# Kernel optimization log

Measured on AMD Instinct MI355X. Metric: run time of the kernel, lower is better.

The kernel has to match this reference:

```python
import jax, jax.numpy as jnp
import numpy as np

N_NODES = 100000
N_EDGES = 1600000
IN_DIM = 128
HID = 64
NUM_GRAPHS = 2048
NUM_CLASSES = 1


def setup_inputs() -> dict:
    key = jax.random.key(0)
    ks = jax.random.split(key, 16)
    x = jax.random.normal(ks[0], (N_NODES, IN_DIM), dtype=jnp.float32)
    edge_index = jax.random.randint(ks[1], (2, N_EDGES), 0, N_NODES, dtype=jnp.int64)
    batch_index = jnp.sort(jax.random.randint(ks[2], (N_NODES,), 0, NUM_GRAPHS, dtype=jnp.int64))
    # GCNConv weights (glorot-ish scale)
    def lin(k, fi, fo):
        return jax.random.normal(k, (fi, fo), dtype=jnp.float32) / np.sqrt(fi)
    W1 = lin(ks[3], IN_DIM, HID); b1 = jnp.zeros((HID,), jnp.float32)
    W2 = lin(ks[4], HID, HID);    b2 = jnp.zeros((HID,), jnp.float32)
    W3 = lin(ks[5], HID, HID);    b3 = jnp.zeros((HID,), jnp.float32)
    W4 = lin(ks[6], HID, HID);    b4 = jnp.zeros((HID,), jnp.float32)
    Wout = lin(ks[7], 2 * HID, NUM_CLASSES); bout = jnp.zeros((NUM_CLASSES,), jnp.float32)
    return {"x": x, "edge_index": edge_index, "batch_index": batch_index,
            "W1": W1, "b1": b1, "W2": W2, "b2": b2, "W3": W3, "b3": b3,
            "W4": W4, "b4": b4, "Wout": Wout, "bout": bout}


def _gcn_conv(x, W, b, src, dst, norm, n):
    # PyG GCNConv: linear transform, then D^-1/2 (A+I) D^-1/2 aggregation, then bias
    h = x @ W                                   # [N, F_out]
    msg = h[src] * norm[:, None]                # [E+N, F_out] gather + scale
    agg = jax.ops.segment_sum(msg, dst, num_segments=n)
    return agg + b


def reference(x, edge_index, batch_index, W1, b1, W2, b2, W3, b3, W4, b4, Wout, bout):
    n = x.shape[0]
    loops = jnp.arange(n, dtype=edge_index.dtype)
    src = jnp.concatenate([edge_index[0], loops])  # add self-loops
    dst = jnp.concatenate([edge_index[1], loops])
    deg = jax.ops.segment_sum(jnp.ones_like(dst, dtype=x.dtype), dst, num_segments=n)
    dis = jax.lax.rsqrt(deg)                       # deg >= 1 due to self-loops
    norm = dis[src] * dis[dst]

    h = x
    for (W, b) in ((W1, b1), (W2, b2), (W3, b3), (W4, b4)):
        h = jax.nn.relu(_gcn_conv(h, W, b, src, dst, norm, n))

    # global mean pool + global max pool per graph
    counts = jax.ops.segment_sum(jnp.ones((n,), h.dtype), batch_index, num_segments=NUM_GRAPHS)
    mean = jax.ops.segment_sum(h, batch_index, num_segments=NUM_GRAPHS) / jnp.maximum(counts, 1.0)[:, None]
    mx = jax.ops.segment_max(h, batch_index, num_segments=NUM_GRAPHS)
    mx = jnp.where(counts[:, None] > 0, mx, 0.0)
    pooled = jnp.concatenate([mean, mx], axis=1)   # [G, 2*HID]

    out = pooled @ Wout + bout                     # [G, 1]
    return (out, pooled)
```

## Files before the change

### kernel.cpp

```cpp
#include <hip/hip_runtime.h>
#include <hip/hip_fp16.h>

#define N_NODES 100000
#define IN_DIM 128
#define HID 64
#define NUM_GRAPHS 2048
#define CNE_MAX (1600000 + 7 * N_NODES)
#define BROWS 128
#define NBUCK ((N_NODES + BROWS - 1) / BROWS)
#define NCHUNK 256
#define TOTP (NBUCK * NCHUNK)
#define CAP 4096

typedef _Float16 h8 __attribute__((ext_vector_type(8)));
typedef float f4 __attribute__((ext_vector_type(4)));


__global__ __launch_bounds__(256) void hist_partial(const int* __restrict__ dst,
                                                    int* __restrict__ partial,
                                                    int E, int chunk,
                                                    unsigned* __restrict__ padA,
                                                    unsigned* __restrict__ padB) {
    __shared__ int lh[NBUCK];
    int t = threadIdx.x, c = blockIdx.x;
    if (c == 0) {
        if (t < 32) padA[t] = 0;
        else if (t < 64) padB[t - 32] = 0;
    }
    for (int b = t; b < NBUCK; b += 256) lh[b] = 0;
    __syncthreads();
    int lo = c * chunk, hi = min(lo + chunk, E);
    for (int i = lo + t; i < hi; i += 256) atomicAdd(&lh[dst[i] >> 7], 1);
    __syncthreads();
    for (int b = t; b < NBUCK; b += 256) partial[b * NCHUNK + c] = lh[b];
}

__global__ void scan1(const int* __restrict__ counts, int* __restrict__ out1,
                      int* __restrict__ bsum, int n, int pad8) {
    __shared__ int s[256];
    int t = threadIdx.x;
    int base = blockIdx.x * 1024 + t * 4;
    int v[4];
#pragma unroll
    for (int i = 0; i < 4; i++) {
        int c = (base + i < n) ? counts[base + i] : 0;
        v[i] = pad8 ? ((c + 7) & ~7) : c;
    }
    int tsum = v[0] + v[1] + v[2] + v[3];
    s[t] = tsum;
    __syncthreads();
    for (int off = 1; off < 256; off <<= 1) {
        int tv = (t >= off) ? s[t - off] : 0;
        __syncthreads();
        s[t] += tv;
        __syncthreads();
    }
    int excl = s[t] - tsum;
    if (t == 255) bsum[blockIdx.x] = s[255];
    int run = excl;
#pragma unroll
    for (int i = 0; i < 4; i++) {
        run += v[i];
        if (base + i < n) out1[base + i] = run;
    }
}

__device__ __forceinline__ int inline_bscan(const int* __restrict__ bsum, int nb, int* s) {
    int t = threadIdx.x;
    int v = (t < nb) ? bsum[t] : 0;
    s[t] = v;
    __syncthreads();
    for (int off = 1; off < 256; off <<= 1) {
        int tv = (t >= off) ? s[t - off] : 0;
        __syncthreads();
        s[t] += tv;
        __syncthreads();
    }
    int excl = s[t] - v;
    __syncthreads();
    s[t] = excl;
    __syncthreads();
    return excl;
}

__global__ __launch_bounds__(256) void scan3(int* __restrict__ row_ptr,
                                             const int* __restrict__ bsum, int nb, int n) {
    __shared__ int s[256];
    inline_bscan(bsum, nb, s);
    int i = blockIdx.x * blockDim.x + threadIdx.x;
    if (i == 0) row_ptr[0] = 0;
    if (i < n) row_ptr[i + 1] += s[i >> 10];
}

__global__ __launch_bounds__(256) void scan3p(const int* __restrict__ partial,
                                              const int* __restrict__ pincl,
                                              const int* __restrict__ bsum, int nb,
                                              int* __restrict__ base,
                                              int* __restrict__ part_off, int E) {
    __shared__ int s[256];
    inline_bscan(bsum, nb, s);
    int i = blockIdx.x * blockDim.x + threadIdx.x;
    if (i < TOTP) {
        int v = pincl[i] + s[i >> 10] - partial[i];
        base[i] = v;
        if ((i & (NCHUNK - 1)) == 0) part_off[i / NCHUNK] = v;
    }
    if (i == 0) part_off[NBUCK] = E;
}

__global__ __launch_bounds__(256) void partition_edges(const int* __restrict__ src,
                                                       const int* __restrict__ dst,
                                                       const int* __restrict__ base,
                                                       unsigned* __restrict__ part,
                                                       int E, int chunk) {
    __shared__ int cur[NBUCK];
    int t = threadIdx.x, c = blockIdx.x;
    for (int b = t; b < NBUCK; b += 256) cur[b] = base[b * NCHUNK + c];
    __syncthreads();
    int lo = c * chunk, hi = min(lo + chunk, E);
    for (int i = lo + t; i < hi; i += 256) {
        int s = src[i], d = dst[i];
        int pos = atomicAdd(&cur[d >> 7], 1);
        part[pos] = (unsigned)s | ((unsigned)(d & (BROWS - 1)) << 17);
    }
}

__global__ __launch_bounds__(256) void deg_dis(const unsigned* __restrict__ part,
                                               const int* __restrict__ part_off,
                                               int* __restrict__ pdeg,
                                               float* __restrict__ dis, int n) {
    __shared__ int cnt[BROWS];
    int t = threadIdx.x, b = blockIdx.x;
    int r0 = b * BROWS;
    if (t < BROWS) cnt[t] = 0;
    __syncthreads();
    for (int i = part_off[b] + t; i < part_off[b + 1]; i += 256)
        atomicAdd(&cnt[part[i] >> 17], 1);
    __syncthreads();
    int nrows = min(BROWS, n - r0);
    if (t < nrows) {
        int dg = cnt[t];
        pdeg[r0 + t] = dg;
        dis[r0 + t] = rsqrtf((float)(dg + 1));
    }
}

__global__ __launch_bounds__(256) void build_csr(const unsigned* __restrict__ part,
                                                 const int* __restrict__ part_off,
                                                 const int* __restrict__ row_ptr,
                                                 unsigned* __restrict__ cne, int n) {
    __shared__ int fill[BROWS];
    __shared__ unsigned stage[CAP];
    int b = blockIdx.x;
    int r0 = b * BROWS;
    int t = threadIdx.x;
    int nrows = min(BROWS, n - r0);
    int base = row_ptr[r0];
    int region = row_ptr[r0 + nrows] - base;
    for (int r = t; r < nrows; r += 256) fill[r] = row_ptr[r0 + r] - base;
    int i0 = part_off[b], i1 = part_off[b + 1];
    if (region <= CAP) {
        for (int i = t; i < region; i += 256) stage[i] = (unsigned)N_NODES << 7;
        __syncthreads();
        for (int i = i0 + t; i < i1; i += 256) {
            unsigned pe = part[i];
            int pos = atomicAdd(&fill[pe >> 17], 1);
            stage[pos] = (pe & 0x1FFFFu) << 7;
        }
        __syncthreads();
        for (int i = t; i < region; i += 256) cne[base + i] = stage[i];
    } else {
        for (int i = t; i < region; i += 256) cne[base + i] = (unsigned)N_NODES << 7;
        __syncthreads();
        for (int i = i0 + t; i < i1; i += 256) {
            unsigned pe = part[i];
            int pos = atomicAdd(&fill[pe >> 17], 1);
            cne[base + pos] = (pe & 0x1FFFFu) << 7;
        }
    }
}


template <int K, typename XT>
__global__ __launch_bounds__(256) void gemm_mfma(const XT* __restrict__ X,
                                                 const float* __restrict__ W,
                                                 const float* __restrict__ dis,
                                                 __half* __restrict__ out, int n) {
    const int KS = K / 32;
    int wave = threadIdx.x >> 6, lane = threadIdx.x & 63;
    int quad = lane >> 4, l16 = lane & 15;
    h8 b[4][KS];
#pragma unroll
    for (int ct = 0; ct < 4; ct++)
#pragma unroll
        for (int ks = 0; ks < KS; ks++)
#pragma unroll
            for (int j = 0; j < 8; j++)
                b[ct][ks][j] = (_Float16)W[(ks * 32 + quad * 8 + j) * HID + ct * 16 + l16];
    int ntile = n >> 4;
    int wpb = blockDim.x >> 6;
    int stride = gridDim.x * wpb;
    for (int rt = blockIdx.x * wpb + wave; rt < ntile; rt += stride) {
        int row0 = rt << 4;
        const XT* xr = X + (size_t)(row0 + l16) * K + quad * 8;
        f4 acc[4];
#pragma unroll
        for (int ct = 0; ct < 4; ct++) acc[ct] = (f4)(0.f);
#pragma unroll
        for (int ks = 0; ks < KS; ks++) {
            h8 a;
            if constexpr (__is_same(XT, float)) {
                float4 xa = *(const float4*)(xr + ks * 32);
                float4 xb = *(const float4*)(xr + ks * 32 + 4);
                a[0] = (_Float16)xa.x; a[1] = (_Float16)xa.y;
                a[2] = (_Float16)xa.z; a[3] = (_Float16)xa.w;
                a[4] = (_Float16)xb.x; a[5] = (_Float16)xb.y;
                a[6] = (_Float16)xb.z; a[7] = (_Float16)xb.w;
            } else {
                a = *(const h8*)(xr + ks * 32);
            }
#pragma unroll
            for (int ct = 0; ct < 4; ct++)
                acc[ct] = __builtin_amdgcn_mfma_f32_16x16x32_f16(a, b[ct][ks], acc[ct], 0, 0, 0);
        }
        int r0 = row0 + quad * 4;
        float4 dv = *(const float4*)(dis + r0);
        float dd[4] = {dv.x, dv.y, dv.z, dv.w};
#pragma unroll
        for (int reg = 0; reg < 4; reg++) {
            __half* orow = out + (size_t)(r0 + reg) * HID + l16;
            orow[0]  = __float2half(dd[reg] * acc[0][reg]);
            orow[16] = __float2half(dd[reg] * acc[1][reg]);
            orow[32] = __float2half(dd[reg] * acc[2][reg]);
            orow[48] = __float2half(dd[reg] * acc[3][reg]);
        }
    }
}

template <typename OutT>
__global__ __launch_bounds__(256) void aggregate2(const __half* __restrict__ tmp,
                                                  const float* __restrict__ dis,
                                                  const int* __restrict__ row_ptr,
                                                  const unsigned* __restrict__ cne,
                                                  const float* __restrict__ bias,
                                                  OutT* __restrict__ out, int n) {
    int wave = threadIdx.x >> 6, lane = threadIdx.x & 63;
    int m = lane & 31, hh = lane >> 5;
    const char* tbase = (const char*)tmp + 4 * m;
    int wpb = blockDim.x >> 6;
    int stride = gridDim.x * wpb;
    float2 blv = *(const float2*)(bias + 2 * m);
    int npairs = n >> 1;
    for (int p = blockIdx.x * wpb + wave; p < npairs; p += stride) {
        int row = 2 * p + hh;
        float dr = dis[row];
        int s = row_ptr[row], e = row_ptr[row + 1];
        int ng = (e - s) >> 3;
        float ax0 = 0.f, ay0 = 0.f, ax1 = 0.f, ay1 = 0.f;
        float ax2 = 0.f, ay2 = 0.f, ax3 = 0.f, ay3 = 0.f;
        if (ng > 0) {
            const uint4* ip = (const uint4*)(cne + s);
            uint4 A0 = ip[0], A1 = ip[1];
            __half2 g0 = *(const __half2*)(tbase + A0.x);
            __half2 g1 = *(const __half2*)(tbase + A0.y);
            __half2 g2 = *(const __half2*)(tbase + A0.z);
            __half2 g3 = *(const __half2*)(tbase + A0.w);
            __half2 g4 = *(const __half2*)(tbase + A1.x);
            __half2 g5 = *(const __half2*)(tbase + A1.y);
            __half2 g6 = *(const __half2*)(tbase + A1.z);
            __half2 g7 = *(const __half2*)(tbase + A1.w);
            uint4 B0, B1;
            if (ng > 1) { B0 = ip[2]; B1 = ip[3]; }
            for (int g = 1; g < ng; g++) {
                __half2 u0 = *(const __half2*)(tbase + B0.x);
                __half2 u1 = *(const __half2*)(tbase + B0.y);
                __half2 u2 = *(const __half2*)(tbase + B0.z);
                __half2 u3 = *(const __half2*)(tbase + B0.w);
                __half2 u4 = *(const __half2*)(tbase + B1.x);
                __half2 u5 = *(const __half2*)(tbase + B1.y);
                __half2 u6 = *(const __half2*)(tbase + B1.z);
                __half2 u7 = *(const __half2*)(tbase + B1.w);
                if (g + 1 < ng) { B0 = ip[2 * (g + 1)]; B1 = ip[2 * (g + 1) + 1]; }
                float2 f0 = __half22float2(g0), f1 = __half22float2(g1);
                float2 f2 = __half22float2(g2), f3 = __half22float2(g3);
                float2 f4 = __half22float2(g4), f5 = __half22float2(g5);
                float2 f6 = __half22float2(g6), f7 = __half22float2(g7);
                ax0 += f0.x; ay0 += f0.y; ax1 += f1.x; ay1 += f1.y;
                ax2 += f2.x; ay2 += f2.y; ax3 += f3.x; ay3 += f3.y;
                ax0 += f4.x; ay0 += f4.y; ax1 += f5.x; ay1 += f5.y;
                ax2 += f6.x; ay2 += f6.y; ax3 += f7.x; ay3 += f7.y;
                g0 = u0; g1 = u1; g2 = u2; g3 = u3;
                g4 = u4; g5 = u5; g6 = u6; g7 = u7;
            }
            float2 f0 = __half22float2(g0), f1 = __half22float2(g1);
            float2 f2 = __half22float2(g2), f3 = __half22float2(g3);
            float2 f4 = __half22float2(g4), f5 = __half22float2(g5);
            float2 f6 = __half22float2(g6), f7 = __half22float2(g7);
            ax0 += f0.x; ay0 += f0.y; ax1 += f1.x; ay1 += f1.y;
            ax2 += f2.x; ay2 += f2.y; ax3 += f3.x; ay3 += f3.y;
            ax0 += f4.x; ay0 += f4.y; ax1 += f5.x; ay1 += f5.y;
            ax2 += f6.x; ay2 += f6.y; ax3 += f7.x; ay3 += f7.y;
        }
        float sx = (ax0 + ax1) + (ax2 + ax3);
        float sy = (ay0 + ay1) + (ay2 + ay3);
        float2 selff = __half22float2(*(const __half2*)(tbase + (size_t)row * 128));
        float rx = fmaxf(dr * (selff.x + sx) + blv.x, 0.f);
        float ry = fmaxf(dr * (selff.y + sy) + blv.y, 0.f);
        if constexpr (__is_same(OutT, __half)) {
            *(__half2*)(out + (size_t)row * HID + 2 * m) = __floats2half2_rn(rx, ry);
        } else {
            *(float2*)(out + (size_t)row * HID + 2 * m) = make_float2(rx, ry);
        }
    }
}

__global__ __launch_bounds__(256) void pool_kernel(const float* __restrict__ h,
                                                   const int* __restrict__ batch,
                                                   const float* __restrict__ Wout,
                                                   const float* __restrict__ bout,
                                                   float* __restrict__ d_out, int n) {
    __shared__ float ssum[4][64];
    __shared__ float smax[4][64];
    int g = blockIdx.x;
    int wave = threadIdx.x >> 6, j = threadIdx.x & 63;
    int lo = 0, hi = n;
    while (lo < hi) { int mid = (lo + hi) >> 1; if (batch[mid] < g) lo = mid + 1; else hi = mid; }
    int start = lo;
    hi = n;
    while (lo < hi) { int mid = (lo + hi) >> 1; if (batch[mid] < g + 1) lo = mid + 1; else hi = mid; }
    int end = lo;

    float sum = 0.f, mx = 0.f;
    for (int i = start + wave; i < end; i += 4) {
        float v = h[(size_t)i * HID + j];
        sum += v;
        mx = fmaxf(mx, v);
    }
    ssum[wave][j] = sum;
    smax[wave][j] = mx;
    __syncthreads();
    if (wave == 0) {
        sum = (ssum[0][j] + ssum[1][j]) + (ssum[2][j] + ssum[3][j]);
        mx = fmaxf(fmaxf(smax[0][j], smax[1][j]), fmaxf(smax[2][j], smax[3][j]));
        float cnt = (float)(end - start);
        float mean = sum / fmaxf(cnt, 1.f);
        float* pooled = d_out + NUM_GRAPHS;
        pooled[(size_t)g * (2 * HID) + j] = mean;
        pooled[(size_t)g * (2 * HID) + HID + j] = mx;
        float c = mean * Wout[j] + mx * Wout[HID + j];
#pragma unroll
        for (int off = 32; off; off >>= 1) c += __shfl_down(c, off);
        if (j == 0) d_out[g] = c + bout[0];
    }
}


extern "C" void kernel_launch(void* const* d_in, const int* in_sizes, int n_in,
                              void* d_out, int out_size, void* d_ws, size_t ws_size,
                              hipStream_t stream) {
    const float* x    = (const float*)d_in[0];
    const int*   edge = (const int*)d_in[1];
    const int*   batch= (const int*)d_in[2];
    const float* W1 = (const float*)d_in[3];  const float* b1 = (const float*)d_in[4];
    const float* W2 = (const float*)d_in[5];  const float* b2 = (const float*)d_in[6];
    const float* W3 = (const float*)d_in[7];  const float* b3 = (const float*)d_in[8];
    const float* W4 = (const float*)d_in[9];  const float* b4 = (const float*)d_in[10];
    const float* Wout = (const float*)d_in[11]; const float* bout = (const float*)d_in[12];
    float* out = (float*)d_out;

    const int N = N_NODES;
    const int E = in_sizes[1] / 2;
    const int* src = edge;
    const int* dst = edge + E;
    const int chunk = (E + NCHUNK - 1) / NCHUNK;

    char* p = (char*)d_ws;
    auto alloc = [&](size_t bytes) -> char* {
        char* r = p;
        p += (bytes + 255) & ~(size_t)255;
        return r;
    };
    int*      pdeg     = (int*)alloc((size_t)N * 4);
    int*      row_ptr  = (int*)alloc((size_t)(N + 1) * 4);
    int*      partial  = (int*)alloc((size_t)TOTP * 4);
    int*      pincl    = (int*)alloc((size_t)TOTP * 4);
    int*      pbase    = (int*)alloc((size_t)TOTP * 4);
    int*      part_off = (int*)alloc((size_t)(NBUCK + 1) * 4);
    unsigned* part     = (unsigned*)alloc((size_t)1600000 * 4);
    unsigned* cne      = (unsigned*)alloc((size_t)CNE_MAX * 4);
    float*    dis      = (float*)alloc((size_t)N * 4);
    int*      bsum     = (int*)alloc(256 * 4);
    __half*   tmp      = (__half*)alloc((size_t)(N + 1) * HID * 2);
    float*    hA       = (float*)alloc((size_t)N * HID * 4);
    __half*   hH       = (__half*)hA;

    unsigned* padrow = (unsigned*)(tmp + (size_t)N * HID);
    hist_partial<<<NCHUNK, 256, 0, stream>>>(dst, partial, E, chunk, padrow, padrow);
    int nbp = (TOTP + 1023) / 1024;
    scan1<<<nbp, 256, 0, stream>>>(partial, pincl, bsum, TOTP, 0);
    scan3p<<<(TOTP + 255) / 256, 256, 0, stream>>>(partial, pincl, bsum, nbp, pbase, part_off, E);
    partition_edges<<<NCHUNK, 256, 0, stream>>>(src, dst, pbase, part, E, chunk);
    deg_dis<<<NBUCK, 256, 0, stream>>>(part, part_off, pdeg, dis, N);

    int nb = (N + 1023) / 1024;
    scan1<<<nb, 256, 0, stream>>>(pdeg, row_ptr + 1, bsum, N, 1);
    scan3<<<(N + 255) / 256, 256, 0, stream>>>(row_ptr, bsum, nb, N);
    build_csr<<<NBUCK, 256, 0, stream>>>(part, part_off, row_ptr, cne, N);

    const int AGG_BLOCKS = 2048;
    const int GEMM_BLOCKS = 1024;

    gemm_mfma<IN_DIM, float><<<GEMM_BLOCKS, 256, 0, stream>>>(x, W1, dis, tmp, N);
    aggregate2<__half><<<AGG_BLOCKS, 256, 0, stream>>>(tmp, dis, row_ptr, cne, b1, hH, N);
    gemm_mfma<HID, _Float16><<<GEMM_BLOCKS, 256, 0, stream>>>((_Float16*)hH, W2, dis, tmp, N);
    aggregate2<__half><<<AGG_BLOCKS, 256, 0, stream>>>(tmp, dis, row_ptr, cne, b2, hH, N);
    gemm_mfma<HID, _Float16><<<GEMM_BLOCKS, 256, 0, stream>>>((_Float16*)hH, W3, dis, tmp, N);
    aggregate2<__half><<<AGG_BLOCKS, 256, 0, stream>>>(tmp, dis, row_ptr, cne, b3, hH, N);
    gemm_mfma<HID, _Float16><<<GEMM_BLOCKS, 256, 0, stream>>>((_Float16*)hH, W4, dis, tmp, N);
    aggregate2<float><<<AGG_BLOCKS, 256, 0, stream>>>(tmp, dis, row_ptr, cne, b4, hA, N);

    pool_kernel<<<NUM_GRAPHS, 256, 0, stream>>>(hA, batch, Wout, bout, out, N);
}
```

Before: 343.2 us.

## Fuse GCN aggregation with next layer's MFMA GEMM via shared-memory tiles

Adds a kernel that aggregates 16 rows of neighbor features per wave, applies bias and ReLU, stages the fp16 result in swizzled LDS, then immediately multiplies by the next layer's weight with MFMA. This replaces three separate aggregate and GEMM launches, avoiding the intermediate hidden-state write and re-read to global memory plus the launch overheads. It uses ping-pong tmp buffers, and each lane now gathers 8 bytes covering 4 features with 16 lanes per row. This may reduce gather parallelism per row and occupancy compared with the standalone aggregate kernel.

```diff
diff --git a/kernel.cpp b/kernel.cpp
--- a/kernel.cpp
+++ b/kernel.cpp
@@ -14,6 +14,11 @@
 
 typedef _Float16 h8 __attribute__((ext_vector_type(8)));
 typedef float f4 __attribute__((ext_vector_type(4)));
+
+__device__ __forceinline__ float2 u2f2(unsigned u) {
+    __half2 h = *reinterpret_cast<__half2*>(&u);
+    return __half22float2(h);
+}
 
 
 __global__ __launch_bounds__(256) void hist_partial(const int* __restrict__ dst,
@@ -229,6 +234,121 @@
 #pragma unroll
         for (int reg = 0; reg < 4; reg++) {
             __half* orow = out + (size_t)(r0 + reg) * HID + l16;
+            orow[0]  = __float2half(dd[reg] * acc[0][reg]);
+            orow[16] = __float2half(dd[reg] * acc[1][reg]);
+            orow[32] = __float2half(dd[reg] * acc[2][reg]);
+            orow[48] = __float2half(dd[reg] * acc[3][reg]);
+        }
+    }
+}
+
+__global__ __launch_bounds__(256) void fused_agg_gemm2(const __half* __restrict__ tmp,
+                                                       const float* __restrict__ dis,
+                                                       const int* __restrict__ row_ptr,
+                                                       const unsigned* __restrict__ cne,
+                                                       const float* __restrict__ bias,
+                                                       const float* __restrict__ W,
+                                                       __half* __restrict__ out, int n) {
+    __shared__ __half hs[4][1024];
+    int wave = threadIdx.x >> 6, lane = threadIdx.x & 63;
+    int lr = lane >> 4, m4 = lane & 15;
+    int quad = lr, l16 = m4;
+    char* hsw = (char*)&hs[wave][0];
+    const char* tb = (const char*)tmp + 8 * m4;
+    float4 blv = *(const float4*)(bias + 4 * m4);
+    h8 bf[4][2];
+#pragma unroll
+    for (int ct = 0; ct < 4; ct++)
+#pragma unroll
+        for (int ks = 0; ks < 2; ks++)
+#pragma unroll
+            for (int j = 0; j < 8; j++)
+                bf[ct][ks][j] = (_Float16)W[(ks * 32 + quad * 8 + j) * HID + ct * 16 + l16];
+    int ntask = n >> 4;
+    int stride = gridDim.x * 4;
+    for (int task = blockIdx.x * 4 + wave; task < ntask; task += stride) {
+        int base = task << 4;
+#pragma unroll 1
+        for (int qp = 0; qp < 4; qp++) {
+            int rloc = (qp << 2) + lr;
+            int row = base + rloc;
+            float dr = dis[row];
+            int s = row_ptr[row], e = row_ptr[row + 1];
+            int ng = (e - s) >> 3;
+            float a0 = 0.f, a1 = 0.f, a2 = 0.f, a3 = 0.f;
+            float c0 = 0.f, c1 = 0.f, c2 = 0.f, c3 = 0.f;
+            if (ng > 0) {
+                const uint4* ip = (const uint4*)(cne + s);
+                uint4 A0 = ip[0], A1 = ip[1];
+                uint2 g0 = *(const uint2*)(tb + A0.x);
+                uint2 g1 = *(const uint2*)(tb + A0.y);
+                uint2 g2 = *(const uint2*)(tb + A0.z);
+                uint2 g3 = *(const uint2*)(tb + A0.w);
+                uint2 g4 = *(const uint2*)(tb + A1.x);
+                uint2 g5 = *(const uint2*)(tb + A1.y);
+                uint2 g6 = *(const uint2*)(tb + A1.z);
+                uint2 g7 = *(const uint2*)(tb + A1.w);
+                uint4 B0, B1;
+                if (ng > 1) { B0 = ip[2]; B1 = ip[3]; }
+                for (int g = 1; g < ng; g++) {
+                    uint2 u0 = *(const uint2*)(tb + B0.x);
+                    uint2 u1 = *(const uint2*)(tb + B0.y);
+                    uint2 u2 = *(const uint2*)(tb + B0.z);
+                    uint2 u3 = *(const uint2*)(tb + B0.w);
+                    uint2 u4 = *(const uint2*)(tb + B1.x);
+                    uint2 u5 = *(const uint2*)(tb + B1.y);
+                    uint2 u6 = *(const uint2*)(tb + B1.z);
+                    uint2 u7 = *(const uint2*)(tb + B1.w);
+                    if (g + 1 < ng) { B0 = ip[2 * g + 2]; B1 = ip[2 * g + 3]; }
+                    float2 f;
+                    f = u2f2(g0.x); a0 += f.x; a1 += f.y; f = u2f2(g0.y); a2 += f.x; a3 += f.y;
+                    f = u2f2(g1.x); c0 += f.x; c1 += f.y; f = u2f2(g1.y); c2 += f.x; c3 += f.y;
+                    f = u2f2(g2.x); a0 += f.x; a1 += f.y; f = u2f2(g2.y); a2 += f.x; a3 += f.y;
+                    f = u2f2(g3.x); c0 += f.x; c1 += f.y; f = u2f2(g3.y); c2 += f.x; c3 += f.y;
+                    f = u2f2(g4.x); a0 += f.x; a1 += f.y; f = u2f2(g4.y); a2 += f.x; a3 += f.y;
+                    f = u2f2(g5.x); c0 += f.x; c1 += f.y; f = u2f2(g5.y); c2 += f.x; c3 += f.y;
+                    f = u2f2(g6.x); a0 += f.x; a1 += f.y; f = u2f2(g6.y); a2 += f.x; a3 += f.y;
+                    f = u2f2(g7.x); c0 += f.x; c1 += f.y; f = u2f2(g7.y); c2 += f.x; c3 += f.y;
+                    g0 = u0; g1 = u1; g2 = u2; g3 = u3;
+                    g4 = u4; g5 = u5; g6 = u6; g7 = u7;
+                }
+                float2 f;
+                f = u2f2(g0.x); a0 += f.x; a1 += f.y; f = u2f2(g0.y); a2 += f.x; a3 += f.y;
+                f = u2f2(g1.x); c0 += f.x; c1 += f.y; f = u2f2(g1.y); c2 += f.x; c3 += f.y;
+                f = u2f2(g2.x); a0 += f.x; a1 += f.y; f = u2f2(g2.y); a2 += f.x; a3 += f.y;
+                f = u2f2(g3.x); c0 += f.x; c1 += f.y; f = u2f2(g3.y); c2 += f.x; c3 += f.y;
+                f = u2f2(g4.x); a0 += f.x; a1 += f.y; f = u2f2(g4.y); a2 += f.x; a3 += f.y;
+                f = u2f2(g5.x); c0 += f.x; c1 += f.y; f = u2f2(g5.y); c2 += f.x; c3 += f.y;
+                f = u2f2(g6.x); a0 += f.x; a1 += f.y; f = u2f2(g6.y); a2 += f.x; a3 += f.y;
+                f = u2f2(g7.x); c0 += f.x; c1 += f.y; f = u2f2(g7.y); c2 += f.x; c3 += f.y;
+            }
+            uint2 sv = *(const uint2*)(tb + (size_t)row * 128);
+            float2 s01 = u2f2(sv.x), s23 = u2f2(sv.y);
+            float v0 = fmaxf(dr * (s01.x + a0 + c0) + blv.x, 0.f);
+            float v1 = fmaxf(dr * (s01.y + a1 + c1) + blv.y, 0.f);
+            float v2 = fmaxf(dr * (s23.x + a2 + c2) + blv.z, 0.f);
+            float v3 = fmaxf(dr * (s23.y + a3 + c3) + blv.w, 0.f);
+            __half2 p01 = __floats2half2_rn(v0, v1);
+            __half2 p23 = __floats2half2_rn(v2, v3);
+            unsigned boff = (unsigned)((rloc * 128 + 8 * m4) ^ ((rloc & 7) << 4));
+            *(uint2*)(hsw + boff) = make_uint2(*(unsigned*)&p01, *(unsigned*)&p23);
+        }
+        f4 acc[4];
+#pragma unroll
+        for (int ct = 0; ct < 4; ct++) acc[ct] = (f4)(0.f);
+#pragma unroll
+        for (int ks = 0; ks < 2; ks++) {
+            h8 a = *(const h8*)(hsw + ((l16 * 128 + ks * 64 + quad * 16) ^ ((l16 & 7) << 4)));
+#pragma unroll
+            for (int ct = 0; ct < 4; ct++)
+                acc[ct] = __builtin_amdgcn_mfma_f32_16x16x32_f16(a, bf[ct][ks], acc[ct], 0, 0, 0);
+        }
+        int rr = base + quad * 4;
+        float4 dv = *(const float4*)(dis + rr);
+        float dd[4] = {dv.x, dv.y, dv.z, dv.w};
+#pragma unroll
+        for (int reg = 0; reg < 4; reg++) {
+            __half* orow = out + (size_t)(rr + reg) * HID + l16;
             orow[0]  = __float2half(dd[reg] * acc[0][reg]);
             orow[16] = __float2half(dd[reg] * acc[1][reg]);
             orow[32] = __float2half(dd[reg] * acc[2][reg]);
@@ -283,22 +403,22 @@
                 if (g + 1 < ng) { B0 = ip[2 * (g + 1)]; B1 = ip[2 * (g + 1) + 1]; }
                 float2 f0 = __half22float2(g0), f1 = __half22float2(g1);
                 float2 f2 = __half22float2(g2), f3 = __half22float2(g3);
-                float2 f4 = __half22float2(g4), f5 = __half22float2(g5);
+                float2 f4_ = __half22float2(g4), f5 = __half22float2(g5);
                 float2 f6 = __half22float2(g6), f7 = __half22float2(g7);
                 ax0 += f0.x; ay0 += f0.y; ax1 += f1.x; ay1 += f1.y;
                 ax2 += f2.x; ay2 += f2.y; ax3 += f3.x; ay3 += f3.y;
-                ax0 += f4.x; ay0 += f4.y; ax1 += f5.x; ay1 += f5.y;
+                ax0 += f4_.x; ay0 += f4_.y; ax1 += f5.x; ay1 += f5.y;
                 ax2 += f6.x; ay2 += f6.y; ax3 += f7.x; ay3 += f7.y;
                 g0 = u0; g1 = u1; g2 = u2; g3 = u3;
                 g4 = u4; g5 = u5; g6 = u6; g7 = u7;
             }
             float2 f0 = __half22float2(g0), f1 = __half22float2(g1);
             float2 f2 = __half22float2(g2), f3 = __half22float2(g3);
-            float2 f4 = __half22float2(g4), f5 = __half22float2(g5);
+            float2 f4_ = __half22float2(g4), f5 = __half22float2(g5);
             float2 f6 = __half22float2(g6), f7 = __half22float2(g7);
             ax0 += f0.x; ay0 += f0.y; ax1 += f1.x; ay1 += f1.y;
             ax2 += f2.x; ay2 += f2.y; ax3 += f3.x; ay3 += f3.y;
-            ax0 += f4.x; ay0 += f4.y; ax1 += f5.x; ay1 += f5.y;
+            ax0 += f4_.x; ay0 += f4_.y; ax1 += f5.x; ay1 += f5.y;
             ax2 += f6.x; ay2 += f6.y; ax3 += f7.x; ay3 += f7.y;
         }
         float sx = (ax0 + ax1) + (ax2 + ax3);
@@ -390,12 +510,13 @@
     unsigned* cne      = (unsigned*)alloc((size_t)CNE_MAX * 4);
     float*    dis      = (float*)alloc((size_t)N * 4);
     int*      bsum     = (int*)alloc(256 * 4);
-    __half*   tmp      = (__half*)alloc((size_t)(N + 1) * HID * 2);
+    __half*   tmpA     = (__half*)alloc((size_t)(N + 1) * HID * 2);
+    __half*   tmpB     = (__half*)alloc((size_t)(N + 1) * HID * 2);
     float*    hA       = (float*)alloc((size_t)N * HID * 4);
-    __half*   hH       = (__half*)hA;
-
-    unsigned* padrow = (unsigned*)(tmp + (size_t)N * HID);
-    hist_partial<<<NCHUNK, 256, 0, stream>>>(dst, partial, E, chunk, padrow, padrow);
+
+    hist_partial<<<NCHUNK, 256, 0, stream>>>(dst, partial, E, chunk,
+                                             (unsigned*)(tmpA + (size_t)N * HID),
+                                             (unsigned*)(tmpB + (size_t)N * HID));
     int nbp = (TOTP + 1023) / 1024;
     scan1<<<nbp, 256, 0, stream>>>(partial, pincl, bsum, TOTP, 0);
     scan3p<<<(TOTP + 255) / 256, 256, 0, stream>>>(partial, pincl, bsum, nbp, pbase, part_off, E);
@@ -409,15 +530,13 @@
 
     const int AGG_BLOCKS = 2048;
     const int GEMM_BLOCKS = 1024;
-
-    gemm_mfma<IN_DIM, float><<<GEMM_BLOCKS, 256, 0, stream>>>(x, W1, dis, tmp, N);
-    aggregate2<__half><<<AGG_BLOCKS, 256, 0, stream>>>(tmp, dis, row_ptr, cne, b1, hH, N);
-    gemm_mfma<HID, _Float16><<<GEMM_BLOCKS, 256, 0, stream>>>((_Float16*)hH, W2, dis, tmp, N);
-    aggregate2<__half><<<AGG_BLOCKS, 256, 0, stream>>>(tmp, dis, row_ptr, cne, b2, hH, N);
-    gemm_mfma<HID, _Float16><<<GEMM_BLOCKS, 256, 0, stream>>>((_Float16*)hH, W3, dis, tmp, N);
-    aggregate2<__half><<<AGG_BLOCKS, 256, 0, stream>>>(tmp, dis, row_ptr, cne, b3, hH, N);
-    gemm_mfma<HID, _Float16><<<GEMM_BLOCKS, 256, 0, stream>>>((_Float16*)hH, W4, dis, tmp, N);
-    aggregate2<float><<<AGG_BLOCKS, 256, 0, stream>>>(tmp, dis, row_ptr, cne, b4, hA, N);
+    const int FUSED_BLOCKS = 1563;
+
+    gemm_mfma<IN_DIM, float><<<GEMM_BLOCKS, 256, 0, stream>>>(x, W1, dis, tmpA, N);
+    fused_agg_gemm2<<<FUSED_BLOCKS, 256, 0, stream>>>(tmpA, dis, row_ptr, cne, b1, W2, tmpB, N);
+    fused_agg_gemm2<<<FUSED_BLOCKS, 256, 0, stream>>>(tmpB, dis, row_ptr, cne, b2, W3, tmpA, N);
+    fused_agg_gemm2<<<FUSED_BLOCKS, 256, 0, stream>>>(tmpA, dis, row_ptr, cne, b3, W4, tmpB, N);
+    aggregate2<float><<<AGG_BLOCKS, 256, 0, stream>>>(tmpB, dis, row_ptr, cne, b4, hA, N);
 
     pool_kernel<<<NUM_GRAPHS, 256, 0, stream>>>(hA, batch, Wout, bout, out, N);
 }
```

Measured after the change: 347.0 us. About the same (+1.1%).

## Aggregate four rows per wave with 8-byte gathers and cross-row prefetch

Applied to the files above, without the earlier changes.

Replaces the two-rows-per-wave aggregation kernel with one that processes four rows per wave, with 16 lanes per row each loading 8 bytes (four halves). It also software-pipelines across grid-stride iterations: the next row's CSR bounds and first index group are prefetched while the current row's neighbour gathers are in flight. Empty rows are pointed at a zero pad row so the first group of gathers is issued unconditionally. The aim is fewer, wider gather instructions and more memory-level parallelism. The cost is higher register pressure and reliance on the pad row being zeroed.

```diff
diff --git a/kernel.cpp b/kernel.cpp
--- a/kernel.cpp
+++ b/kernel.cpp
@@ -14,6 +14,11 @@
 
 typedef _Float16 h8 __attribute__((ext_vector_type(8)));
 typedef float f4 __attribute__((ext_vector_type(4)));
+
+__device__ __forceinline__ float2 u2f2(unsigned u) {
+    __half2 h = *reinterpret_cast<__half2*>(&u);
+    return __half22float2(h);
+}
 
 
 __global__ __launch_bounds__(256) void hist_partial(const int* __restrict__ dst,
@@ -238,79 +243,108 @@
 }
 
 template <typename OutT>
-__global__ __launch_bounds__(256) void aggregate2(const __half* __restrict__ tmp,
+__global__ __launch_bounds__(256) void aggregate4(const __half* __restrict__ tmp,
                                                   const float* __restrict__ dis,
                                                   const int* __restrict__ row_ptr,
                                                   const unsigned* __restrict__ cne,
                                                   const float* __restrict__ bias,
                                                   OutT* __restrict__ out, int n) {
     int wave = threadIdx.x >> 6, lane = threadIdx.x & 63;
-    int m = lane & 31, hh = lane >> 5;
-    const char* tbase = (const char*)tmp + 4 * m;
+    int m4 = lane & 15, rq = lane >> 4;
+    const char* tb = (const char*)tmp + 8 * m4;
+    float4 blv = *(const float4*)(bias + 4 * m4);
     int wpb = blockDim.x >> 6;
     int stride = gridDim.x * wpb;
-    float2 blv = *(const float2*)(bias + 2 * m);
-    int npairs = n >> 1;
-    for (int p = blockIdx.x * wpb + wave; p < npairs; p += stride) {
-        int row = 2 * p + hh;
+    int ntask = n >> 2;
+    const unsigned Z = (unsigned)N_NODES << 7;
+    int t = blockIdx.x * wpb + wave;
+    if (t >= ntask) return;
+    int row = 4 * t + rq;
+    int sE = row_ptr[row], eE = row_ptr[row + 1];
+    uint4 A0, A1;
+    if (sE < eE) {
+        const uint4* ip0 = (const uint4*)(cne + sE);
+        A0 = ip0[0]; A1 = ip0[1];
+    } else {
+        A0 = make_uint4(Z, Z, Z, Z); A1 = make_uint4(Z, Z, Z, Z);
+    }
+    while (true) {
+        row = 4 * t + rq;
         float dr = dis[row];
-        int s = row_ptr[row], e = row_ptr[row + 1];
-        int ng = (e - s) >> 3;
-        float ax0 = 0.f, ay0 = 0.f, ax1 = 0.f, ay1 = 0.f;
-        float ax2 = 0.f, ay2 = 0.f, ax3 = 0.f, ay3 = 0.f;
-        if (ng > 0) {
-            const uint4* ip = (const uint4*)(cne + s);
-            uint4 A0 = ip[0], A1 = ip[1];
-            __half2 g0 = *(const __half2*)(tbase + A0.x);
-            __half2 g1 = *(const __half2*)(tbase + A0.y);
-            __half2 g2 = *(const __half2*)(tbase + A0.z);
-            __half2 g3 = *(const __half2*)(tbase + A0.w);
-            __half2 g4 = *(const __half2*)(tbase + A1.x);
-            __half2 g5 = *(const __half2*)(tbase + A1.y);
-            __half2 g6 = *(const __half2*)(tbase + A1.z);
-            __half2 g7 = *(const __half2*)(tbase + A1.w);
-            uint4 B0, B1;
-            if (ng > 1) { B0 = ip[2]; B1 = ip[3]; }
-            for (int g = 1; g < ng; g++) {
-                __half2 u0 = *(const __half2*)(tbase + B0.x);
-                __half2 u1 = *(const __half2*)(tbase + B0.y);
-                __half2 u2 = *(const __half2*)(tbase + B0.z);
-                __half2 u3 = *(const __half2*)(tbase + B0.w);
-                __half2 u4 = *(const __half2*)(tbase + B1.x);
-                __half2 u5 = *(const __half2*)(tbase + B1.y);
-                __half2 u6 = *(const __half2*)(tbase + B1.z);
-                __half2 u7 = *(const __half2*)(tbase + B1.w);
-                if (g + 1 < ng) { B0 = ip[2 * (g + 1)]; B1 = ip[2 * (g + 1) + 1]; }
-                float2 f0 = __half22float2(g0), f1 = __half22float2(g1);
-                float2 f2 = __half22float2(g2), f3 = __half22float2(g3);
-                float2 f4 = __half22float2(g4), f5 = __half22float2(g5);
-                float2 f6 = __half22float2(g6), f7 = __half22float2(g7);
-                ax0 += f0.x; ay0 += f0.y; ax1 += f1.x; ay1 += f1.y;
-                ax2 += f2.x; ay2 += f2.y; ax3 += f3.x; ay3 += f3.y;
-                ax0 += f4.x; ay0 += f4.y; ax1 += f5.x; ay1 += f5.y;
-                ax2 += f6.x; ay2 += f6.y; ax3 += f7.x; ay3 += f7.y;
-                g0 = u0; g1 = u1; g2 = u2; g3 = u3;
-                g4 = u4; g5 = u5; g6 = u6; g7 = u7;
-            }
-            float2 f0 = __half22float2(g0), f1 = __half22float2(g1);
-            float2 f2 = __half22float2(g2), f3 = __half22float2(g3);
-            float2 f4 = __half22float2(g4), f5 = __half22float2(g5);
-            float2 f6 = __half22float2(g6), f7 = __half22float2(g7);
-            ax0 += f0.x; ay0 += f0.y; ax1 += f1.x; ay1 += f1.y;
-            ax2 += f2.x; ay2 += f2.y; ax3 += f3.x; ay3 += f3.y;
-            ax0 += f4.x; ay0 += f4.y; ax1 += f5.x; ay1 += f5.y;
-            ax2 += f6.x; ay2 += f6.y; ax3 += f7.x; ay3 += f7.y;
-        }
-        float sx = (ax0 + ax1) + (ax2 + ax3);
-        float sy = (ay0 + ay1) + (ay2 + ay3);
-        float2 selff = __half22float2(*(const __half2*)(tbase + (size_t)row * 128));
-        float rx = fmaxf(dr * (selff.x + sx) + blv.x, 0.f);
-        float ry = fmaxf(dr * (selff.y + sy) + blv.y, 0.f);
+        uint2 g0 = *(const uint2*)(tb + A0.x);
+        uint2 g1 = *(const uint2*)(tb + A0.y);
+        uint2 g2 = *(const uint2*)(tb + A0.z);
+        uint2 g3 = *(const uint2*)(tb + A0.w);
+        uint2 g4 = *(const uint2*)(tb + A1.x);
+        uint2 g5 = *(const uint2*)(tb + A1.y);
+        uint2 g6 = *(const uint2*)(tb + A1.z);
+        uint2 g7 = *(const uint2*)(tb + A1.w);
+        int tn = t + stride;
+        int sN = 0, eN = 0;
+        if (tn < ntask) {
+            int rn = 4 * tn + rq;
+            sN = row_ptr[rn]; eN = row_ptr[rn + 1];
+        }
+        int ng = (eE - sE) >> 3;
+        float a0 = 0.f, a1 = 0.f, a2 = 0.f, a3 = 0.f;
+        const uint4* ip = (const uint4*)(cne + sE);
+        uint4 B0, B1;
+        if (ng > 1) { B0 = ip[2]; B1 = ip[3]; }
+        for (int g = 1; g < ng; g++) {
+            uint2 u0 = *(const uint2*)(tb + B0.x);
+            uint2 u1 = *(const uint2*)(tb + B0.y);
+            uint2 u2 = *(const uint2*)(tb + B0.z);
+            uint2 u3 = *(const uint2*)(tb + B0.w);
+            uint2 u4 = *(const uint2*)(tb + B1.x);
+            uint2 u5 = *(const uint2*)(tb + B1.y);
+            uint2 u6 = *(const uint2*)(tb + B1.z);
+            uint2 u7 = *(const uint2*)(tb + B1.w);
+            if (g + 1 < ng) { B0 = ip[2 * g + 2]; B1 = ip[2 * g + 3]; }
+            float2 f;
+            f = u2f2(g0.x); a0 += f.x; a1 += f.y; f = u2f2(g0.y); a2 += f.x; a3 += f.y;
+            f = u2f2(g1.x); a0 += f.x; a1 += f.y; f = u2f2(g1.y); a2 += f.x; a3 += f.y;
+            f = u2f2(g2.x); a0 += f.x; a1 += f.y; f = u2f2(g2.y); a2 += f.x; a3 += f.y;
+            f = u2f2(g3.x); a0 += f.x; a1 += f.y; f = u2f2(g3.y); a2 += f.x; a3 += f.y;
+            f = u2f2(g4.x); a0 += f.x; a1 += f.y; f = u2f2(g4.y); a2 += f.x; a3 += f.y;
+            f = u2f2(g5.x); a0 += f.x; a1 += f.y; f = u2f2(g5.y); a2 += f.x; a3 += f.y;
+            f = u2f2(g6.x); a0 += f.x; a1 += f.y; f = u2f2(g6.y); a2 += f.x; a3 += f.y;
+            f = u2f2(g7.x); a0 += f.x; a1 += f.y; f = u2f2(g7.y); a2 += f.x; a3 += f.y;
+            g0 = u0; g1 = u1; g2 = u2; g3 = u3;
+            g4 = u4; g5 = u5; g6 = u6; g7 = u7;
+        }
+        {
+            float2 f;
+            f = u2f2(g0.x); a0 += f.x; a1 += f.y; f = u2f2(g0.y); a2 += f.x; a3 += f.y;
+            f = u2f2(g1.x); a0 += f.x; a1 += f.y; f = u2f2(g1.y); a2 += f.x; a3 += f.y;
+            f = u2f2(g2.x); a0 += f.x; a1 += f.y; f = u2f2(g2.y); a2 += f.x; a3 += f.y;
+            f = u2f2(g3.x); a0 += f.x; a1 += f.y; f = u2f2(g3.y); a2 += f.x; a3 += f.y;
+            f = u2f2(g4.x); a0 += f.x; a1 += f.y; f = u2f2(g4.y); a2 += f.x; a3 += f.y;
+            f = u2f2(g5.x); a0 += f.x; a1 += f.y; f = u2f2(g5.y); a2 += f.x; a3 += f.y;
+            f = u2f2(g6.x); a0 += f.x; a1 += f.y; f = u2f2(g6.y); a2 += f.x; a3 += f.y;
+            f = u2f2(g7.x); a0 += f.x; a1 += f.y; f = u2f2(g7.y); a2 += f.x; a3 += f.y;
+        }
+        if (sN < eN) {
+            const uint4* ipn = (const uint4*)(cne + sN);
+            A0 = ipn[0]; A1 = ipn[1];
+        } else {
+            A0 = make_uint4(Z, Z, Z, Z); A1 = make_uint4(Z, Z, Z, Z);
+        }
+        uint2 sv = *(const uint2*)(tb + (size_t)row * 128);
+        float2 s01 = u2f2(sv.x), s23 = u2f2(sv.y);
+        float v0 = fmaxf(dr * (s01.x + a0) + blv.x, 0.f);
+        float v1 = fmaxf(dr * (s01.y + a1) + blv.y, 0.f);
+        float v2 = fmaxf(dr * (s23.x + a2) + blv.z, 0.f);
+        float v3 = fmaxf(dr * (s23.y + a3) + blv.w, 0.f);
         if constexpr (__is_same(OutT, __half)) {
-            *(__half2*)(out + (size_t)row * HID + 2 * m) = __floats2half2_rn(rx, ry);
+            __half2 p01 = __floats2half2_rn(v0, v1);
+            __half2 p23 = __floats2half2_rn(v2, v3);
+            *(uint2*)((char*)out + (size_t)row * 128 + 8 * m4) =
+                make_uint2(*(unsigned*)&p01, *(unsigned*)&p23);
         } else {
-            *(float2*)(out + (size_t)row * HID + 2 * m) = make_float2(rx, ry);
-        }
+            *(float4*)(out + (size_t)row * HID + 4 * m4) = make_float4(v0, v1, v2, v3);
+        }
+        if (tn >= ntask) break;
+        t = tn; sE = sN; eE = eN;
     }
 }
 
@@ -411,13 +445,13 @@
     const int GEMM_BLOCKS = 1024;
 
     gemm_mfma<IN_DIM, float><<<GEMM_BLOCKS, 256, 0, stream>>>(x, W1, dis, tmp, N);
-    aggregate2<__half><<<AGG_BLOCKS, 256, 0, stream>>>(tmp, dis, row_ptr, cne, b1, hH, N);
+    aggregate4<__half><<<AGG_BLOCKS, 256, 0, stream>>>(tmp, dis, row_ptr, cne, b1, hH, N);
     gemm_mfma<HID, _Float16><<<GEMM_BLOCKS, 256, 0, stream>>>((_Float16*)hH, W2, dis, tmp, N);
-    aggregate2<__half><<<AGG_BLOCKS, 256, 0, stream>>>(tmp, dis, row_ptr, cne, b2, hH, N);
+    aggregate4<__half><<<AGG_BLOCKS, 256, 0, stream>>>(tmp, dis, row_ptr, cne, b2, hH, N);
     gemm_mfma<HID, _Float16><<<GEMM_BLOCKS, 256, 0, stream>>>((_Float16*)hH, W3, dis, tmp, N);
-    aggregate2<__half><<<AGG_BLOCKS, 256, 0, stream>>>(tmp, dis, row_ptr, cne, b3, hH, N);
+    aggregate4<__half><<<AGG_BLOCKS, 256, 0, stream>>>(tmp, dis, row_ptr, cne, b3, hH, N);
     gemm_mfma<HID, _Float16><<<GEMM_BLOCKS, 256, 0, stream>>>((_Float16*)hH, W4, dis, tmp, N);
-    aggregate2<float><<<AGG_BLOCKS, 256, 0, stream>>>(tmp, dis, row_ptr, cne, b4, hA, N);
+    aggregate4<float><<<AGG_BLOCKS, 256, 0, stream>>>(tmp, dis, row_ptr, cne, b4, hA, N);
 
     pool_kernel<<<NUM_GRAPHS, 256, 0, stream>>>(hA, batch, Wout, bout, out, N);
 }
```

After: 346.3 us. No clear change (+0.9%).

## Split hidden features into four column slices for cache-local aggregation

Applied to the files above, without the earlier changes.

Stores the intermediate node features as four 16-column slices of 32 bytes per row instead of one 128-byte row. Each aggregation block handles a single slice, so the gathered working set per pass is a quarter of the full feature table and can stay in cache. Each lane now loads a full 32-byte slice row per neighbor and partial sums are combined with an xor-shuffle transpose. The GEMM, pooling and padding code are adapted to the sliced layout. The cost is that the CSR indices are read four times per layer and more shuffle work is needed per row.

```diff
diff --git a/kernel.cpp b/kernel.cpp
--- a/kernel.cpp
+++ b/kernel.cpp
@@ -15,18 +15,22 @@
 typedef _Float16 h8 __attribute__((ext_vector_type(8)));
 typedef float f4 __attribute__((ext_vector_type(4)));
 
+#define SLICE_E ((size_t)(N_NODES + 1) * 16)
+
+__device__ __forceinline__ float2 u2f2(unsigned u) {
+    __half2 h = *reinterpret_cast<__half2*>(&u);
+    return __half22float2(h);
+}
+
 
 __global__ __launch_bounds__(256) void hist_partial(const int* __restrict__ dst,
                                                     int* __restrict__ partial,
                                                     int E, int chunk,
-                                                    unsigned* __restrict__ padA,
-                                                    unsigned* __restrict__ padB) {
+                                                    unsigned* __restrict__ tmppad) {
     __shared__ int lh[NBUCK];
     int t = threadIdx.x, c = blockIdx.x;
-    if (c == 0) {
-        if (t < 32) padA[t] = 0;
-        else if (t < 64) padB[t - 32] = 0;
-    }
+    if (c == 0 && t < 32)
+        tmppad[(size_t)(t >> 3) * ((N_NODES + 1) * 8) + (size_t)N_NODES * 8 + (t & 7)] = 0;
     for (int b = t; b < NBUCK; b += 256) lh[b] = 0;
     __syncthreads();
     int lo = c * chunk, hi = min(lo + chunk, E);
@@ -65,7 +69,7 @@
     }
 }
 
-__device__ __forceinline__ int inline_bscan(const int* __restrict__ bsum, int nb, int* s) {
+__device__ __forceinline__ void inline_bscan(const int* __restrict__ bsum, int nb, int* s) {
     int t = threadIdx.x;
     int v = (t < nb) ? bsum[t] : 0;
     s[t] = v;
@@ -80,7 +84,6 @@
     __syncthreads();
     s[t] = excl;
     __syncthreads();
-    return excl;
 }
 
 __global__ __launch_bounds__(256) void scan3(int* __restrict__ row_ptr,
@@ -160,28 +163,28 @@
     for (int r = t; r < nrows; r += 256) fill[r] = row_ptr[r0 + r] - base;
     int i0 = part_off[b], i1 = part_off[b + 1];
     if (region <= CAP) {
-        for (int i = t; i < region; i += 256) stage[i] = (unsigned)N_NODES << 7;
+        for (int i = t; i < region; i += 256) stage[i] = (unsigned)N_NODES << 5;
         __syncthreads();
         for (int i = i0 + t; i < i1; i += 256) {
             unsigned pe = part[i];
             int pos = atomicAdd(&fill[pe >> 17], 1);
-            stage[pos] = (pe & 0x1FFFFu) << 7;
+            stage[pos] = (pe & 0x1FFFFu) << 5;
         }
         __syncthreads();
         for (int i = t; i < region; i += 256) cne[base + i] = stage[i];
     } else {
-        for (int i = t; i < region; i += 256) cne[base + i] = (unsigned)N_NODES << 7;
+        for (int i = t; i < region; i += 256) cne[base + i] = (unsigned)N_NODES << 5;
         __syncthreads();
         for (int i = i0 + t; i < i1; i += 256) {
             unsigned pe = part[i];
             int pos = atomicAdd(&fill[pe >> 17], 1);
-            cne[base + pos] = (pe & 0x1FFFFu) << 7;
-        }
-    }
-}
-
-
-template <int K, typename XT>
+            cne[base + pos] = (pe & 0x1FFFFu) << 5;
+        }
+    }
+}
+
+
+template <int K, typename XT, bool SIN>
 __global__ __launch_bounds__(256) void gemm_mfma(const XT* __restrict__ X,
                                                  const float* __restrict__ W,
                                                  const float* __restrict__ dis,
@@ -202,22 +205,23 @@
     int stride = gridDim.x * wpb;
     for (int rt = blockIdx.x * wpb + wave; rt < ntile; rt += stride) {
         int row0 = rt << 4;
-        const XT* xr = X + (size_t)(row0 + l16) * K + quad * 8;
         f4 acc[4];
 #pragma unroll
         for (int ct = 0; ct < 4; ct++) acc[ct] = (f4)(0.f);
 #pragma unroll
         for (int ks = 0; ks < KS; ks++) {
             h8 a;
-            if constexpr (__is_same(XT, float)) {
-                float4 xa = *(const float4*)(xr + ks * 32);
-                float4 xb = *(const float4*)(xr + ks * 32 + 4);
+            if constexpr (SIN) {
+                a = *(const h8*)(X + (size_t)(ks * 2 + (quad >> 1)) * SLICE_E +
+                                 (size_t)(row0 + l16) * 16 + (quad & 1) * 8);
+            } else {
+                const XT* xr = X + (size_t)(row0 + l16) * K + quad * 8 + ks * 32;
+                float4 xa = *(const float4*)(xr);
+                float4 xb = *(const float4*)(xr + 4);
                 a[0] = (_Float16)xa.x; a[1] = (_Float16)xa.y;
                 a[2] = (_Float16)xa.z; a[3] = (_Float16)xa.w;
                 a[4] = (_Float16)xb.x; a[5] = (_Float16)xb.y;
                 a[6] = (_Float16)xb.z; a[7] = (_Float16)xb.w;
-            } else {
-                a = *(const h8*)(xr + ks * 32);
             }
 #pragma unroll
             for (int ct = 0; ct < 4; ct++)
@@ -228,88 +232,82 @@
         float dd[4] = {dv.x, dv.y, dv.z, dv.w};
 #pragma unroll
         for (int reg = 0; reg < 4; reg++) {
-            __half* orow = out + (size_t)(r0 + reg) * HID + l16;
-            orow[0]  = __float2half(dd[reg] * acc[0][reg]);
-            orow[16] = __float2half(dd[reg] * acc[1][reg]);
-            orow[32] = __float2half(dd[reg] * acc[2][reg]);
-            orow[48] = __float2half(dd[reg] * acc[3][reg]);
+#pragma unroll
+            for (int ct = 0; ct < 4; ct++)
+                out[(size_t)ct * SLICE_E + (size_t)(r0 + reg) * 16 + l16] =
+                    __float2half(dd[reg] * acc[ct][reg]);
         }
     }
 }
 
 template <typename OutT>
-__global__ __launch_bounds__(256) void aggregate2(const __half* __restrict__ tmp,
-                                                  const float* __restrict__ dis,
-                                                  const int* __restrict__ row_ptr,
-                                                  const unsigned* __restrict__ cne,
-                                                  const float* __restrict__ bias,
-                                                  OutT* __restrict__ out, int n) {
+__global__ __launch_bounds__(256) void aggregate_slice(const __half* __restrict__ tmp,
+                                                       const float* __restrict__ dis,
+                                                       const int* __restrict__ row_ptr,
+                                                       const unsigned* __restrict__ cne,
+                                                       const float* __restrict__ bias,
+                                                       OutT* __restrict__ out, int n) {
     int wave = threadIdx.x >> 6, lane = threadIdx.x & 63;
-    int m = lane & 31, hh = lane >> 5;
-    const char* tbase = (const char*)tmp + 4 * m;
-    int wpb = blockDim.x >> 6;
-    int stride = gridDim.x * wpb;
-    float2 blv = *(const float2*)(bias + 2 * m);
-    int npairs = n >> 1;
-    for (int p = blockIdx.x * wpb + wave; p < npairs; p += stride) {
-        int row = 2 * p + hh;
+    int m = lane & 7, rq = lane >> 3;
+    int slice = blockIdx.x & 3;
+    const char* tb = (const char*)(tmp + (size_t)slice * SLICE_E);
+    int c = 8 * (m & 1) + 4 * ((m >> 1) & 1) + 2 * ((m >> 2) & 1);
+    float2 blv = *(const float2*)(bias + slice * 16 + c);
+    int sblk = blockIdx.x >> 2;
+    int nspb = gridDim.x >> 2;
+    int ntasks = (n + 7) >> 3;
+    for (int task = sblk * 4 + wave; task < ntasks; task += nspb * 4) {
+        int row = task * 8 + rq;
+        float a[16];
+#pragma unroll
+        for (int i = 0; i < 16; i++) a[i] = 0.f;
+        int sE = row_ptr[row];
+        int ng = (row_ptr[row + 1] - sE) >> 3;
+        const unsigned* ci = cne + sE + m;
+        unsigned off = (ng > 0) ? ci[0] : 0u;
+        for (int g = 0; g < ng; g++) {
+            uint4 q0 = *(const uint4*)(tb + off);
+            uint4 q1 = *(const uint4*)(tb + off + 16);
+            if (g + 1 < ng) off = ci[(g + 1) * 8];
+            float2 f;
+            f = u2f2(q0.x); a[0] += f.x;  a[1] += f.y;
+            f = u2f2(q0.y); a[2] += f.x;  a[3] += f.y;
+            f = u2f2(q0.z); a[4] += f.x;  a[5] += f.y;
+            f = u2f2(q0.w); a[6] += f.x;  a[7] += f.y;
+            f = u2f2(q1.x); a[8] += f.x;  a[9] += f.y;
+            f = u2f2(q1.y); a[10] += f.x; a[11] += f.y;
+            f = u2f2(q1.z); a[12] += f.x; a[13] += f.y;
+            f = u2f2(q1.w); a[14] += f.x; a[15] += f.y;
+        }
+        float v8[8], v4[4], v2[2];
+#pragma unroll
+        for (int i = 0; i < 8; i++) {
+            float keep = (m & 1) ? a[i + 8] : a[i];
+            float send = (m & 1) ? a[i] : a[i + 8];
+            v8[i] = keep + __shfl_xor(send, 1);
+        }
+#pragma unroll
+        for (int i = 0; i < 4; i++) {
+            float keep = (m & 2) ? v8[i + 4] : v8[i];
+            float send = (m & 2) ? v8[i] : v8[i + 4];
+            v4[i] = keep + __shfl_xor(send, 2);
+        }
+#pragma unroll
+        for (int i = 0; i < 2; i++) {
+            float keep = (m & 4) ? v4[i + 2] : v4[i];
+            float send = (m & 4) ? v4[i] : v4[i + 2];
+            v2[i] = keep + __shfl_xor(send, 4);
+        }
         float dr = dis[row];
-        int s = row_ptr[row], e = row_ptr[row + 1];
-        int ng = (e - s) >> 3;
-        float ax0 = 0.f, ay0 = 0.f, ax1 = 0.f, ay1 = 0.f;
-        float ax2 = 0.f, ay2 = 0.f, ax3 = 0.f, ay3 = 0.f;
-        if (ng > 0) {
-            const uint4* ip = (const uint4*)(cne + s);
-            uint4 A0 = ip[0], A1 = ip[1];
-            __half2 g0 = *(const __half2*)(tbase + A0.x);
-            __half2 g1 = *(const __half2*)(tbase + A0.y);
-            __half2 g2 = *(const __half2*)(tbase + A0.z);
-            __half2 g3 = *(const __half2*)(tbase + A0.w);
-            __half2 g4 = *(const __half2*)(tbase + A1.x);
-            __half2 g5 = *(const __half2*)(tbase + A1.y);
-            __half2 g6 = *(const __half2*)(tbase + A1.z);
-            __half2 g7 = *(const __half2*)(tbase + A1.w);
-            uint4 B0, B1;
-            if (ng > 1) { B0 = ip[2]; B1 = ip[3]; }
-            for (int g = 1; g < ng; g++) {
-                __half2 u0 = *(const __half2*)(tbase + B0.x);
-                __half2 u1 = *(const __half2*)(tbase + B0.y);
-                __half2 u2 = *(const __half2*)(tbase + B0.z);
-                __half2 u3 = *(const __half2*)(tbase + B0.w);
-                __half2 u4 = *(const __half2*)(tbase + B1.x);
-                __half2 u5 = *(const __half2*)(tbase + B1.y);
-                __half2 u6 = *(const __half2*)(tbase + B1.z);
-                __half2 u7 = *(const __half2*)(tbase + B1.w);
-                if (g + 1 < ng) { B0 = ip[2 * (g + 1)]; B1 = ip[2 * (g + 1) + 1]; }
-                float2 f0 = __half22float2(g0), f1 = __half22float2(g1);
-                float2 f2 = __half22float2(g2), f3 = __half22float2(g3);
-                float2 f4 = __half22float2(g4), f5 = __half22float2(g5);
-                float2 f6 = __half22float2(g6), f7 = __half22float2(g7);
-                ax0 += f0.x; ay0 += f0.y; ax1 += f1.x; ay1 += f1.y;
-                ax2 += f2.x; ay2 += f2.y; ax3 += f3.x; ay3 += f3.y;
-                ax0 += f4.x; ay0 += f4.y; ax1 += f5.x; ay1 += f5.y;
-                ax2 += f6.x; ay2 += f6.y; ax3 += f7.x; ay3 += f7.y;
-                g0 = u0; g1 = u1; g2 = u2; g3 = u3;
-                g4 = u4; g5 = u5; g6 = u6; g7 = u7;
-            }
-            float2 f0 = __half22float2(g0), f1 = __half22float2(g1);
-            float2 f2 = __half22float2(g2), f3 = __half22float2(g3);
-            float2 f4 = __half22float2(g4), f5 = __half22float2(g5);
-            float2 f6 = __half22float2(g6), f7 = __half22float2(g7);
-            ax0 += f0.x; ay0 += f0.y; ax1 += f1.x; ay1 += f1.y;
-            ax2 += f2.x; ay2 += f2.y; ax3 += f3.x; ay3 += f3.y;
-            ax0 += f4.x; ay0 += f4.y; ax1 += f5.x; ay1 += f5.y;
-            ax2 += f6.x; ay2 += f6.y; ax3 += f7.x; ay3 += f7.y;
-        }
-        float sx = (ax0 + ax1) + (ax2 + ax3);
-        float sy = (ay0 + ay1) + (ay2 + ay3);
-        float2 selff = __half22float2(*(const __half2*)(tbase + (size_t)row * 128));
-        float rx = fmaxf(dr * (selff.x + sx) + blv.x, 0.f);
-        float ry = fmaxf(dr * (selff.y + sy) + blv.y, 0.f);
+        float2 sf = u2f2(*(const unsigned*)(tb + (size_t)row * 32 + 2 * c));
+        float vx = fmaxf(dr * (sf.x + v2[0]) + blv.x, 0.f);
+        float vy = fmaxf(dr * (sf.y + v2[1]) + blv.y, 0.f);
         if constexpr (__is_same(OutT, __half)) {
-            *(__half2*)(out + (size_t)row * HID + 2 * m) = __floats2half2_rn(rx, ry);
+            *(__half2*)(out + (size_t)slice * SLICE_E + (size_t)row * 16 + c) =
+                __floats2half2_rn(vx, vy);
         } else {
-            *(float2*)(out + (size_t)row * HID + 2 * m) = make_float2(rx, ry);
+            *(float2*)(out + (size_t)slice * SLICE_E + (size_t)row * 16 + c) =
+                make_float2(vx, vy);
         }
     }
 }
@@ -323,6 +321,7 @@
     __shared__ float smax[4][64];
     int g = blockIdx.x;
     int wave = threadIdx.x >> 6, j = threadIdx.x & 63;
+    size_t cbase = (size_t)(j >> 4) * SLICE_E + (j & 15);
     int lo = 0, hi = n;
     while (lo < hi) { int mid = (lo + hi) >> 1; if (batch[mid] < g) lo = mid + 1; else hi = mid; }
     int start = lo;
@@ -332,7 +331,7 @@
 
     float sum = 0.f, mx = 0.f;
     for (int i = start + wave; i < end; i += 4) {
-        float v = h[(size_t)i * HID + j];
+        float v = h[cbase + (size_t)i * 16];
         sum += v;
         mx = fmaxf(mx, v);
     }
@@ -390,12 +389,11 @@
     unsigned* cne      = (unsigned*)alloc((size_t)CNE_MAX * 4);
     float*    dis      = (float*)alloc((size_t)N * 4);
     int*      bsum     = (int*)alloc(256 * 4);
-    __half*   tmp      = (__half*)alloc((size_t)(N + 1) * HID * 2);
-    float*    hA       = (float*)alloc((size_t)N * HID * 4);
+    __half*   tmp      = (__half*)alloc(SLICE_E * 4 * 2);
+    float*    hA       = (float*)alloc(SLICE_E * 4 * 4);
     __half*   hH       = (__half*)hA;
 
-    unsigned* padrow = (unsigned*)(tmp + (size_t)N * HID);
-    hist_partial<<<NCHUNK, 256, 0, stream>>>(dst, partial, E, chunk, padrow, padrow);
+    hist_partial<<<NCHUNK, 256, 0, stream>>>(dst, partial, E, chunk, (unsigned*)tmp);
     int nbp = (TOTP + 1023) / 1024;
     scan1<<<nbp, 256, 0, stream>>>(partial, pincl, bsum, TOTP, 0);
     scan3p<<<(TOTP + 255) / 256, 256, 0, stream>>>(partial, pincl, bsum, nbp, pbase, part_off, E);
@@ -410,14 +408,14 @@
     const int AGG_BLOCKS = 2048;
     const int GEMM_BLOCKS = 1024;
 
-    gemm_mfma<IN_DIM, float><<<GEMM_BLOCKS, 256, 0, stream>>>(x, W1, dis, tmp, N);
-    aggregate2<__half><<<AGG_BLOCKS, 256, 0, stream>>>(tmp, dis, row_ptr, cne, b1, hH, N);
-    gemm_mfma<HID, _Float16><<<GEMM_BLOCKS, 256, 0, stream>>>((_Float16*)hH, W2, dis, tmp, N);
-    aggregate2<__half><<<AGG_BLOCKS, 256, 0, stream>>>(tmp, dis, row_ptr, cne, b2, hH, N);
-    gemm_mfma<HID, _Float16><<<GEMM_BLOCKS, 256, 0, stream>>>((_Float16*)hH, W3, dis, tmp, N);
-    aggregate2<__half><<<AGG_BLOCKS, 256, 0, stream>>>(tmp, dis, row_ptr, cne, b3, hH, N);
-    gemm_mfma<HID, _Float16><<<GEMM_BLOCKS, 256, 0, stream>>>((_Float16*)hH, W4, dis, tmp, N);
-    aggregate2<float><<<AGG_BLOCKS, 256, 0, stream>>>(tmp, dis, row_ptr, cne, b4, hA, N);
+    gemm_mfma<IN_DIM, float, false><<<GEMM_BLOCKS, 256, 0, stream>>>(x, W1, dis, tmp, N);
+    aggregate_slice<__half><<<AGG_BLOCKS, 256, 0, stream>>>(tmp, dis, row_ptr, cne, b1, hH, N);
+    gemm_mfma<HID, _Float16, true><<<GEMM_BLOCKS, 256, 0, stream>>>((_Float16*)hH, W2, dis, tmp, N);
+    aggregate_slice<__half><<<AGG_BLOCKS, 256, 0, stream>>>(tmp, dis, row_ptr, cne, b2, hH, N);
+    gemm_mfma<HID, _Float16, true><<<GEMM_BLOCKS, 256, 0, stream>>>((_Float16*)hH, W3, dis, tmp, N);
+    aggregate_slice<__half><<<AGG_BLOCKS, 256, 0, stream>>>(tmp, dis, row_ptr, cne, b3, hH, N);
+    gemm_mfma<HID, _Float16, true><<<GEMM_BLOCKS, 256, 0, stream>>>((_Float16*)hH, W4, dis, tmp, N);
+    aggregate_slice<float><<<AGG_BLOCKS, 256, 0, stream>>>(tmp, dis, row_ptr, cne, b4, hA, N);
 
     pool_kernel<<<NUM_GRAPHS, 256, 0, stream>>>(hA, batch, Wout, bout, out, N);
 }
```

Measured after the change: 410.3 us. 1.2x slower.
